# Kernel optimization log

Measured on AMD Instinct MI355X. Metric: run time of the kernel, lower is better.

The kernel has to match this reference:

```python
import jax, jax.numpy as jnp
import numpy as np

NUM_CLASSES = 6
EPS = 1e-10


def setup_inputs() -> dict:
    key = jax.random.key(0)
    k1, k2 = jax.random.split(key)
    latent = jax.random.normal(k1, (8192, 128), dtype=jnp.float32)
    label = jax.random.randint(k2, (8192,), 0, NUM_CLASSES, dtype=jnp.int64)
    return {"latent": latent, "label": label}


def reference(latent, label):
    # Full pairwise cosine similarity: S[a,b] = <x_a, x_b> / max(|x_a||x_b|, eps)
    # (matches torch.nn.CosineSimilarity's per-pair clamped denominator)
    norms = jnp.linalg.norm(latent, axis=1)                      # [B]
    dots = latent @ latent.T                                      # [B, B]
    S = dots / jnp.maximum(norms[:, None] * norms[None, :], EPS)  # [B, B]

    # Per-class-pair block sums: P[i,j] = sum_{a in class i, b in class j} S[a,b]
    onehot = jax.nn.one_hot(label, NUM_CLASSES, dtype=latent.dtype)  # [B, C]
    P = onehot.T @ S @ onehot                                        # [C, C]
    counts = jnp.sum(onehot, axis=0)                                 # [C]

    # Original divides block (i,j) by max(1, n_i^2 - n_i) (uses first class's size)
    denom = jnp.maximum(counts * counts - counts, 1.0)               # [C]
    iu, ju = jnp.triu_indices(NUM_CLASSES, k=1)
    dists = P[iu, ju] / denom[iu]
    return jnp.mean(dists)
```

## Files before the change

### kernel.cpp

```cpp
#include <hip/hip_runtime.h>

#define BATCH 8192
#define DIM 128
#define NCLS 6
#define NPAIRS 15
#define NBLK 128
#define NTHR 512
#define WPB (NTHR / 64)
#define NWAVES (NBLK * WPB)
#define NPAIRROWS (BATCH / 2)
#define ZLEN (NCLS * DIM)


__global__ __launch_bounds__(NTHR) void class_sum_kernel(
    const float* __restrict__ latent,
    const int* __restrict__ label,
    float* __restrict__ gpart,
    float* __restrict__ gcntp)
{
    __shared__ float lz[WPB][ZLEN];
    __shared__ int   lcnt[WPB][NCLS];

    const int tid  = threadIdx.x;
    const int lane = tid & 63;
    const int w    = tid >> 6;
    const int half = lane >> 5;
    const int hl   = lane & 31;
    const int gw   = blockIdx.x * WPB + w;

    float4 acc[NCLS];
    int    cnt[NCLS];
    #pragma unroll
    for (int c = 0; c < NCLS; ++c) { acc[c] = make_float4(0.f, 0.f, 0.f, 0.f); cnt[c] = 0; }

    for (int pair = gw; pair < NPAIRROWS; pair += NWAVES) {
        const int row = pair * 2 + half;
        const float4 v = *reinterpret_cast<const float4*>(
            latent + (size_t)row * DIM + hl * 4);
        float ss = v.x * v.x + v.y * v.y + v.z * v.z + v.w * v.w;
        #pragma unroll
        for (int off = 16; off >= 1; off >>= 1)
            ss += __shfl_xor(ss, off);
        const float rn = 1.0f / sqrtf(ss);
        const int lab = label[row];
        #pragma unroll
        for (int c = 0; c < NCLS; ++c) {
            const float m = (lab == c) ? rn : 0.0f;
            acc[c].x += v.x * m;  acc[c].y += v.y * m;
            acc[c].z += v.z * m;  acc[c].w += v.w * m;
            cnt[c]   += (hl == 0) ? (int)(lab == c) : 0;
        }
    }

    #pragma unroll
    for (int c = 0; c < NCLS; ++c) {
        acc[c].x += __shfl_xor(acc[c].x, 32);
        acc[c].y += __shfl_xor(acc[c].y, 32);
        acc[c].z += __shfl_xor(acc[c].z, 32);
        acc[c].w += __shfl_xor(acc[c].w, 32);
        cnt[c]   += __shfl_xor(cnt[c], 32);
    }

    if (lane < 32) {
        #pragma unroll
        for (int c = 0; c < NCLS; ++c)
            *reinterpret_cast<float4*>(&lz[w][c * DIM + lane * 4]) = acc[c];
    }
    if (lane == 0) {
        #pragma unroll
        for (int c = 0; c < NCLS; ++c) lcnt[w][c] = cnt[c];
    }
    __syncthreads();

    for (int e = tid; e < ZLEN; e += NTHR) {
        float s = 0.f;
        #pragma unroll
        for (int ww = 0; ww < WPB; ++ww) s += lz[ww][e];
        gpart[blockIdx.x * ZLEN + e] = s;
    }
    if (tid < NCLS) {
        int s = 0;
        #pragma unroll
        for (int ww = 0; ww < WPB; ++ww) s += lcnt[ww][tid];
        gcntp[blockIdx.x * NCLS + tid] = (float)s;
    }
}

__global__ __launch_bounds__(1024) void finalize_kernel(
    const float* __restrict__ gpart,
    const float* __restrict__ gcntp,
    float* __restrict__ out)
{
    __shared__ float zz[ZLEN];
    __shared__ float cf[NCLS];
    __shared__ float ps[NPAIRS];
    const int tid = threadIdx.x;

    if (tid < ZLEN) {
        float s = 0.f;
        for (int b = 0; b < NBLK; ++b) s += gpart[b * ZLEN + tid];
        zz[tid] = s;
    } else if (tid < ZLEN + NCLS) {
        const int c = tid - ZLEN;
        float s = 0.f;
        for (int b = 0; b < NBLK; ++b) s += gcntp[b * NCLS + c];
        cf[c] = s;
    } else if (tid < ZLEN + NCLS + NPAIRS) {
        ps[tid - ZLEN - NCLS] = 0.f;
    }
    __syncthreads();

    if (tid < DIM) {
        float zi[NCLS];
        #pragma unroll
        for (int c = 0; c < NCLS; ++c) zi[c] = zz[c * DIM + tid];
        int p = 0;
        #pragma unroll
        for (int i = 0; i < NCLS; ++i) {
            #pragma unroll
            for (int j = i + 1; j < NCLS; ++j, ++p)
                atomicAdd(&ps[p], zi[i] * zi[j]);
        }
    }
    __syncthreads();

    if (tid == 0) {
        float acc = 0.f;
        int p = 0;
        for (int i = 0; i < NCLS; ++i) {
            const float n = cf[i];
            const float denom = fmaxf(n * n - n, 1.0f);
            for (int j = i + 1; j < NCLS; ++j, ++p)
                acc += ps[p] / denom;
        }
        out[0] = acc / (float)NPAIRS;
    }
}

extern "C" void kernel_launch(void* const* d_in, const int* in_sizes, int n_in,
                              void* d_out, int out_size, void* d_ws, size_t ws_size,
                              hipStream_t stream) {
    const float* latent = (const float*)d_in[0];
    const int* label = (const int*)d_in[1];
    float* out = (float*)d_out;

    float* gpart = (float*)d_ws;
    float* gcntp = gpart + NBLK * ZLEN;

    class_sum_kernel<<<NBLK, NTHR, 0, stream>>>(latent, label, gpart, gcntp);
    finalize_kernel<<<1, 1024, 0, stream>>>(gpart, gcntp, out);
}
```

Before: 43.97 us.

## Fuse class-sum and finalize into one cooperative kernel with grid sync

Merges the two kernels into one cooperative launch that uses a grid-wide barrier before block 0 does the final reduction. This removes the second kernel launch and its launch gap. It also halves the grid to 64 blocks, which shortens the finalize reduction but gives each wave more rows. It adds unroll hints as well. Cooperative launch and grid sync bring their own overhead.

```diff
diff --git a/kernel.cpp b/kernel.cpp
--- a/kernel.cpp
+++ b/kernel.cpp
@@ -1,10 +1,11 @@
 #include <hip/hip_runtime.h>
+#include <hip/hip_cooperative_groups.h>
 
 #define BATCH 8192
 #define DIM 128
 #define NCLS 6
 #define NPAIRS 15
-#define NBLK 128
+#define NBLK 64
 #define NTHR 512
 #define WPB (NTHR / 64)
 #define NWAVES (NBLK * WPB)
@@ -12,11 +13,12 @@
 #define ZLEN (NCLS * DIM)
 
 
-__global__ __launch_bounds__(NTHR) void class_sum_kernel(
+__global__ __launch_bounds__(NTHR) void fused_kernel(
     const float* __restrict__ latent,
     const int* __restrict__ label,
     float* __restrict__ gpart,
-    float* __restrict__ gcntp)
+    float* __restrict__ gcntp,
+    float* __restrict__ out)
 {
     __shared__ float lz[WPB][ZLEN];
     __shared__ int   lcnt[WPB][NCLS];
@@ -33,6 +35,7 @@
     #pragma unroll
     for (int c = 0; c < NCLS; ++c) { acc[c] = make_float4(0.f, 0.f, 0.f, 0.f); cnt[c] = 0; }
 
+    #pragma unroll 2
     for (int pair = gw; pair < NPAIRROWS; pair += NWAVES) {
         const int row = pair * 2 + half;
         const float4 v = *reinterpret_cast<const float4*>(
@@ -84,30 +87,28 @@
         for (int ww = 0; ww < WPB; ++ww) s += lcnt[ww][tid];
         gcntp[blockIdx.x * NCLS + tid] = (float)s;
     }
-}
 
-__global__ __launch_bounds__(1024) void finalize_kernel(
-    const float* __restrict__ gpart,
-    const float* __restrict__ gcntp,
-    float* __restrict__ out)
-{
+    cooperative_groups::this_grid().sync();
+
+    if (blockIdx.x != 0) return;
+
     __shared__ float zz[ZLEN];
     __shared__ float cf[NCLS];
     __shared__ float ps[NPAIRS];
-    const int tid = threadIdx.x;
 
-    if (tid < ZLEN) {
+    for (int e = tid; e < ZLEN; e += NTHR) {
         float s = 0.f;
-        for (int b = 0; b < NBLK; ++b) s += gpart[b * ZLEN + tid];
-        zz[tid] = s;
-    } else if (tid < ZLEN + NCLS) {
-        const int c = tid - ZLEN;
+        #pragma unroll 8
+        for (int b = 0; b < NBLK; ++b) s += gpart[b * ZLEN + e];
+        zz[e] = s;
+    }
+    if (tid < NCLS) {
         float s = 0.f;
-        for (int b = 0; b < NBLK; ++b) s += gcntp[b * NCLS + c];
-        cf[c] = s;
-    } else if (tid < ZLEN + NCLS + NPAIRS) {
-        ps[tid - ZLEN - NCLS] = 0.f;
+        #pragma unroll 8
+        for (int b = 0; b < NBLK; ++b) s += gcntp[b * NCLS + tid];
+        cf[tid] = s;
     }
+    if (tid >= NTHR - NPAIRS) ps[tid - (NTHR - NPAIRS)] = 0.f;
     __syncthreads();
 
     if (tid < DIM) {
@@ -125,15 +126,15 @@
     __syncthreads();
 
     if (tid == 0) {
-        float acc = 0.f;
+        float acc2 = 0.f;
         int p = 0;
         for (int i = 0; i < NCLS; ++i) {
             const float n = cf[i];
             const float denom = fmaxf(n * n - n, 1.0f);
             for (int j = i + 1; j < NCLS; ++j, ++p)
-                acc += ps[p] / denom;
+                acc2 += ps[p] / denom;
         }
-        out[0] = acc / (float)NPAIRS;
+        out[0] = acc2 / (float)NPAIRS;
     }
 }
 
@@ -147,6 +148,8 @@
     float* gpart = (float*)d_ws;
     float* gcntp = gpart + NBLK * ZLEN;
 
-    class_sum_kernel<<<NBLK, NTHR, 0, stream>>>(latent, label, gpart, gcntp);
-    finalize_kernel<<<1, 1024, 0, stream>>>(gpart, gcntp, out);
+    void* args[] = { (void*)&latent, (void*)&label, (void*)&gpart,
+                     (void*)&gcntp, (void*)&out };
+    hipLaunchCooperativeKernel((void*)fused_kernel, dim3(NBLK), dim3(NTHR),
+                               args, 0, stream);
 }
```

After: 71.93 us. 1.64x slower.
